# Kernel optimization log

Measured on AMD Instinct MI355X. Metric: run time of the kernel, lower is better.

The kernel has to match this reference:

```python
import jax, jax.numpy as jnp
import numpy as np

B, S, D = 4, 2048, 1024
H = 16
DH = D // H

def setup_inputs() -> dict:
    key = jax.random.key(0)
    ks = jax.random.split(key, 5)
    s = 1.0 / np.sqrt(D)
    return {
        "inputs": jax.random.normal(ks[0], (B, S, D), dtype=jnp.float32),
        "Wq": jax.random.normal(ks[1], (D, D), dtype=jnp.float32) * s,
        "Wk": jax.random.normal(ks[2], (D, D), dtype=jnp.float32) * s,
        "Wv": jax.random.normal(ks[3], (D, D), dtype=jnp.float32) * s,
        "Wo": jax.random.normal(ks[4], (D, D), dtype=jnp.float32) * s,
        "bo": jnp.zeros((D,), dtype=jnp.float32),
    }

def reference(inputs, Wq, Wk, Wv, Wo, bo):
    b, s, _ = inputs.shape
    # nn.Linear: y = x @ W.T (no bias for QKV)
    Q = (inputs @ Wq.T).reshape(b, s, H, DH)
    K = (inputs @ Wk.T).reshape(b, s, H, DH)
    V = (inputs @ Wv.T).reshape(b, s, H, DH)
    scores = jnp.einsum("bqhd,bkhd->bhqk", Q, K)  # [B,H,S,S]
    causal = jnp.triu(jnp.ones((s, s), dtype=bool), k=1)
    scores = jnp.where(causal, -jnp.inf, scores)
    w = jax.nn.softmax(scores / np.sqrt(DH), axis=-1)  # dropout p=0.0 -> identity
    Z = jnp.einsum("bhqk,bkhd->bqhd", w, V).reshape(b, s, D)
    return Z @ Wo.T + bo
```

## Files before the change

kernel.cpp:

```cpp
#include <hip/hip_runtime.h>
#include <hip/hip_bf16.h>


#define Bq 4
#define Sq 2048
#define Dq 1024
#define Hq 16
#define DHq 64

typedef __attribute__((ext_vector_type(8))) short short8;
typedef __attribute__((ext_vector_type(4))) float f32x4;
typedef __attribute__((ext_vector_type(4))) unsigned short ushort4v;
typedef __attribute__((ext_vector_type(2))) unsigned int uint2v;

static __device__ __forceinline__ unsigned short f2bfu(float f) {
    union { __hip_bfloat16 h; unsigned short u; } cv;
    cv.h = __float2bfloat16(f);
    return cv.u;
}
static __device__ __forceinline__ unsigned int cvtpk(float lo, float hi) {
    unsigned int r;
    asm("v_cvt_pk_bf16_f32 %0, %1, %2" : "=v"(r) : "v"(lo), "v"(hi));
    return r;
}

__global__ __launch_bounds__(256) void tobf16(
    const float* __restrict__ X, const float* __restrict__ W0,
    const float* __restrict__ W1, const float* __restrict__ W2,
    const float* __restrict__ W3,
    unsigned short* __restrict__ xb, unsigned short* __restrict__ wb)
{
    const size_t i = ((size_t)blockIdx.x * 256 + threadIdx.x) * 8;
    const size_t NX = (size_t)8388608;
    const float* src; unsigned short* dst; size_t off;
    if (i < NX) { src = X; dst = xb; off = i; }
    else {
        const size_t j = i - NX;
        const int w = (int)(j >> 20);
        off = j & 1048575;
        src = (w == 0) ? W0 : (w == 1) ? W1 : (w == 2) ? W2 : W3;
        dst = wb + ((size_t)w << 20);
    }
    const float4 a = *reinterpret_cast<const float4*>(src + off);
    const float4 b = *reinterpret_cast<const float4*>(src + off + 4);
    short8 v;
    v[0] = (short)f2bfu(a.x); v[1] = (short)f2bfu(a.y);
    v[2] = (short)f2bfu(a.z); v[3] = (short)f2bfu(a.w);
    v[4] = (short)f2bfu(b.x); v[5] = (short)f2bfu(b.y);
    v[6] = (short)f2bfu(b.z); v[7] = (short)f2bfu(b.w);
    *reinterpret_cast<short8*>(dst + off) = v;
}



__global__ __launch_bounds__(256) void mm_qkv(
    const unsigned short* __restrict__ Ab, const unsigned short* __restrict__ Wall,
    unsigned short* __restrict__ oq, unsigned short* __restrict__ ok,
    unsigned short* __restrict__ ovt)
{
    __shared__ unsigned short As[128 * 64];
    __shared__ unsigned short Bs[128 * 64];

    const int z = blockIdx.z;
    const unsigned short* W = Wall + ((size_t)z << 20);

    const int m0 = blockIdx.x * 128, n0 = blockIdx.y * 128;
    const int t = threadIdx.x, lane = t & 63, wave = t >> 6;
    const int g = lane >> 4, c = lane & 15;
    const int wm = wave >> 1, wn = wave & 1;
    const int r8 = lane >> 3, c8 = lane & 7;
    const int ss = (c8 ^ (r8 & 7)) * 8;

    f32x4 acc[4][4] = {};

    for (int kt = 0; kt < 16; ++kt) {
        const int kb = kt * 64;
#pragma unroll
        for (int p = 0; p < 4; ++p) {
            const int rowb = wave * 8 + p * 32;
            const unsigned short* ga = Ab + (size_t)(m0 + rowb + r8) * 1024 + kb + ss;
            const unsigned short* gb = W  + (size_t)(n0 + rowb + r8) * 1024 + kb + ss;
            __builtin_amdgcn_global_load_lds(
                (const __attribute__((address_space(1))) unsigned int*)ga,
                (__attribute__((address_space(3))) unsigned int*)(As + rowb * 64), 16, 0, 0);
            __builtin_amdgcn_global_load_lds(
                (const __attribute__((address_space(1))) unsigned int*)gb,
                (__attribute__((address_space(3))) unsigned int*)(Bs + rowb * 64), 16, 0, 0);
        }
        __syncthreads();
        if (z != 2) {
#pragma unroll
            for (int ks = 0; ks < 2; ++ks) {
                const int sa = ((ks * 4 + g) ^ (c & 7)) * 8;
                short8 bf[4];
#pragma unroll
                for (int nt = 0; nt < 4; ++nt)
                    bf[nt] = *reinterpret_cast<const short8*>(&Bs[(wn * 64 + nt * 16 + c) * 64 + sa]);
#pragma unroll
                for (int mt = 0; mt < 4; ++mt) {
                    const short8 af = *reinterpret_cast<const short8*>(&As[(wm * 64 + mt * 16 + c) * 64 + sa]);
#pragma unroll
                    for (int nt = 0; nt < 4; ++nt)
                        acc[mt][nt] = __builtin_amdgcn_mfma_f32_16x16x32_bf16(af, bf[nt], acc[mt][nt], 0, 0, 0);
                }
            }
        } else {
#pragma unroll
            for (int ks = 0; ks < 2; ++ks) {
                const int sa = ((ks * 4 + g) ^ (c & 7)) * 8;
                short8 bf[4];
#pragma unroll
                for (int nt = 0; nt < 4; ++nt)
                    bf[nt] = *reinterpret_cast<const short8*>(&Bs[(wn * 64 + nt * 16 + c) * 64 + sa]);
#pragma unroll
                for (int mt = 0; mt < 4; ++mt) {
                    const short8 af = *reinterpret_cast<const short8*>(&As[(wm * 64 + mt * 16 + c) * 64 + sa]);
#pragma unroll
                    for (int nt = 0; nt < 4; ++nt)
                        acc[mt][nt] = __builtin_amdgcn_mfma_f32_16x16x32_bf16(bf[nt], af, acc[mt][nt], 0, 0, 0);
                }
            }
        }
        __syncthreads();
    }

    if (z == 2) {
#pragma unroll
        for (int mt = 0; mt < 4; ++mt)
#pragma unroll
            for (int nt = 0; nt < 4; ++nt)
#pragma unroll
                for (int r = 0; r < 4; ++r) {
                    const int m = m0 + wm * 64 + mt * 16 + c;
                    const int n = n0 + wn * 64 + nt * 16 + g * 4 + r;
                    const int bb = m >> 11, s = m & 2047;
                    const int h = n >> 6, d = n & 63;
                    const size_t off = (size_t)(bb * Hq + h) * 131072
                        + (s >> 6) * 4096 + ((d >> 4) & 3) * 1024 + ((s >> 5) & 1) * 512
                        + ((s >> 3) & 3) * 128 + (d & 15) * 8 + (s & 7);
                    ovt[off] = f2bfu(acc[mt][nt][r]);
                }
    } else {
        const float oscale = (z == 0) ? 0.180336880f : 1.0f;
        unsigned short* out = z ? ok : oq;
#pragma unroll
        for (int mt = 0; mt < 4; ++mt)
#pragma unroll
            for (int nt = 0; nt < 4; ++nt)
#pragma unroll
                for (int r = 0; r < 4; ++r) {
                    const int m = m0 + wm * 64 + mt * 16 + g * 4 + r;
                    const int n = n0 + wn * 64 + nt * 16 + c;
                    const int bb = m >> 11, s = m & 2047;
                    const int h = n >> 6, d = n & 63;
                    const size_t off = (size_t)(bb * Hq + h) * 131072
                        + (s >> 4) * 1024 + (d >> 5) * 512 + ((d >> 3) & 3) * 128
                        + (s & 15) * 8 + (d & 7);
                    out[off] = f2bfu(acc[mt][nt][r] * oscale);
                }
    }
}

static __device__ __forceinline__ void stage_kv8(
    const unsigned short* __restrict__ Kb, const unsigned short* __restrict__ Vb,
    int kb, unsigned short* kl, unsigned short* vl, int wave, int lane)
{
    const int off = wave * 512 + lane * 8;
    __builtin_amdgcn_global_load_lds(
        (const __attribute__((address_space(1))) unsigned int*)(Kb + (size_t)kb * 4096 + off),
        (__attribute__((address_space(3))) unsigned int*)(kl + wave * 512), 16, 0, 0);
    __builtin_amdgcn_global_load_lds(
        (const __attribute__((address_space(1))) unsigned int*)(Vb + (size_t)kb * 4096 + off),
        (__attribute__((address_space(3))) unsigned int*)(vl + wave * 512), 16, 0, 0);
}

static __device__ __forceinline__ void pack_p(
    f32x4* st, int rel, int g, int c, unsigned short (*PtW)[72],
    short8& pb0, short8& pb1)
{
    if (rel < 4) {
        const int lim = rel * 16 + c;
#pragma unroll
        for (int kt = 0; kt < 4; ++kt)
#pragma unroll
            for (int r = 0; r < 4; ++r)
                if (kt * 16 + g * 4 + r > lim) st[kt][r] = -3.0e38f;
    }
#pragma unroll
    for (int kt = 0; kt < 4; ++kt) {
        uint2v u;
        u[0] = cvtpk(exp2f(st[kt][0]), exp2f(st[kt][1]));
        u[1] = cvtpk(exp2f(st[kt][2]), exp2f(st[kt][3]));
        *reinterpret_cast<uint2v*>(&PtW[c][kt * 16 + g * 4]) = u;
    }
    pb0 = *reinterpret_cast<const short8*>(&PtW[c][g * 8]);
    pb1 = *reinterpret_cast<const short8*>(&PtW[c][32 + g * 8]);
}

__global__ __launch_bounds__(512, 2) void attn(
    const unsigned short* __restrict__ Qf, const unsigned short* __restrict__ Kf,
    const unsigned short* __restrict__ Vf, unsigned short* __restrict__ O)
{
    __shared__ unsigned short Kl[2][4096];
    __shared__ unsigned short Vl[2][4096];
    __shared__ unsigned short Pt[8][16][72];

    const int bid = blockIdx.x;
    const int half = bid >> 8;
    const int idx = (bid >> 6) & 3;
    const int qq = half ? (3 - idx) : (4 + idx);
    const int bh = (bid & 7) | (((bid >> 3) & 7) << 3);

    const int t = threadIdx.x, lane = t & 63, wave = t >> 6;
    const int g = lane >> 4, c = lane & 15;
    const size_t base = (size_t)bh * (Sq * DHq);
    const unsigned short* Qb = Qf + base;
    const unsigned short* Kb = Kf + base;
    const unsigned short* Vb = Vf + base;
    const int b = bh >> 4, h = bh & 15;

    short8 onesf;
#pragma unroll
    for (int j = 0; j < 8; ++j) onesf[j] = (short)0x3F80;

    const int qtA = qq * 16 + wave * 2;
    const int qtB = qtA + 1;

    const unsigned short* qpA = Qb + (size_t)qtA * 1024 + lane * 8;
    const unsigned short* qpB = Qb + (size_t)qtB * 1024 + lane * 8;
    const short8 qA0 = *reinterpret_cast<const short8*>(qpA);
    const short8 qA1 = *reinterpret_cast<const short8*>(qpA + 512);
    const short8 qB0 = *reinterpret_cast<const short8*>(qpB);
    const short8 qB1 = *reinterpret_cast<const short8*>(qpB + 512);

    f32x4 oA[4] = {}, oB[4] = {};
    f32x4 lA = {}, lB = {};

    const int ibmax = 4 * qq + 3;

    stage_kv8(Kb, Vb, 0, Kl[0], Vl[0], wave, lane);
    __syncthreads();

#pragma unroll 1
    for (int ib = 0; ib <= ibmax; ++ib) {
        const int cur = ib & 1;
        if (ib < ibmax)
            stage_kv8(Kb, Vb, ib + 1, Kl[cur ^ 1], Vl[cur ^ 1], wave, lane);
        __builtin_amdgcn_sched_barrier(0);

        if (4 * ib <= qtA) {
            const unsigned short* kl = &Kl[cur][lane * 8];
            const unsigned short* vl = &Vl[cur][lane * 8];

            f32x4 stA[4] = {}, stB[4] = {};
#pragma unroll
            for (int k2 = 0; k2 < 4; ++k2) {
                const short8 kf0 = *reinterpret_cast<const short8*>(&kl[(2 * k2) * 512]);
                const short8 kf1 = *reinterpret_cast<const short8*>(&kl[(2 * k2 + 1) * 512]);
                stA[k2] = __builtin_amdgcn_mfma_f32_16x16x32_bf16(kf0, qA0, stA[k2], 0, 0, 0);
                stA[k2] = __builtin_amdgcn_mfma_f32_16x16x32_bf16(kf1, qA1, stA[k2], 0, 0, 0);
                stB[k2] = __builtin_amdgcn_mfma_f32_16x16x32_bf16(kf0, qB0, stB[k2], 0, 0, 0);
                stB[k2] = __builtin_amdgcn_mfma_f32_16x16x32_bf16(kf1, qB1, stB[k2], 0, 0, 0);
            }

            short8 pbA0, pbA1, pbB0, pbB1;
            pack_p(stA, qtA - 4 * ib, g, c, Pt[wave], pbA0, pbA1);
            pack_p(stB, qtB - 4 * ib, g, c, Pt[wave], pbB0, pbB1);

            lA = __builtin_amdgcn_mfma_f32_16x16x32_bf16(onesf, pbA0, lA, 0, 0, 0);
            lA = __builtin_amdgcn_mfma_f32_16x16x32_bf16(onesf, pbA1, lA, 0, 0, 0);
            lB = __builtin_amdgcn_mfma_f32_16x16x32_bf16(onesf, pbB0, lB, 0, 0, 0);
            lB = __builtin_amdgcn_mfma_f32_16x16x32_bf16(onesf, pbB1, lB, 0, 0, 0);

#pragma unroll
            for (int dt = 0; dt < 4; ++dt) {
                const short8 vf0 = *reinterpret_cast<const short8*>(&vl[(2 * dt) * 512]);
                const short8 vf1 = *reinterpret_cast<const short8*>(&vl[(2 * dt + 1) * 512]);
                oA[dt] = __builtin_amdgcn_mfma_f32_16x16x32_bf16(vf0, pbA0, oA[dt], 0, 0, 0);
                oA[dt] = __builtin_amdgcn_mfma_f32_16x16x32_bf16(vf1, pbA1, oA[dt], 0, 0, 0);
                oB[dt] = __builtin_amdgcn_mfma_f32_16x16x32_bf16(vf0, pbB0, oB[dt], 0, 0, 0);
                oB[dt] = __builtin_amdgcn_mfma_f32_16x16x32_bf16(vf1, pbB1, oB[dt], 0, 0, 0);
            }
        }
        __syncthreads();
    }

    const float rlA = 1.0f / lA[0];
    const float rlB = 1.0f / lB[0];
    const size_t orowA = ((size_t)b * Sq + qtA * 16 + c) * Dq + h * 64;
    const size_t orowB = ((size_t)b * Sq + qtB * 16 + c) * Dq + h * 64;
#pragma unroll
    for (int dt = 0; dt < 4; ++dt) {
        uint2v uA, uB;
        uA[0] = cvtpk(oA[dt][0] * rlA, oA[dt][1] * rlA);
        uA[1] = cvtpk(oA[dt][2] * rlA, oA[dt][3] * rlA);
        uB[0] = cvtpk(oB[dt][0] * rlB, oB[dt][1] * rlB);
        uB[1] = cvtpk(oB[dt][2] * rlB, oB[dt][3] * rlB);
        *reinterpret_cast<uint2v*>(&O[orowA + dt * 16 + g * 4]) = uA;
        *reinterpret_cast<uint2v*>(&O[orowB + dt * 16 + g * 4]) = uB;
    }
}

__global__ __launch_bounds__(256) void mm_o(
    const unsigned short* __restrict__ Ab, const unsigned short* __restrict__ Wall,
    const float* __restrict__ bo, float* __restrict__ outf)
{
    __shared__ unsigned short As[128 * 64];
    __shared__ unsigned short Bs[128 * 64];

    const unsigned short* W = Wall + ((size_t)3 << 20);

    const int m0 = blockIdx.x * 128, n0 = blockIdx.y * 128;
    const int t = threadIdx.x, lane = t & 63, wave = t >> 6;
    const int g = lane >> 4, c = lane & 15;
    const int wm = wave >> 1, wn = wave & 1;
    const int r8 = lane >> 3, c8 = lane & 7;
    const int ss = (c8 ^ (r8 & 7)) * 8;

    f32x4 acc[4][4] = {};

    for (int kt = 0; kt < 16; ++kt) {
        const int kb = kt * 64;
#pragma unroll
        for (int p = 0; p < 4; ++p) {
            const int rowb = wave * 8 + p * 32;
            const unsigned short* ga = Ab + (size_t)(m0 + rowb + r8) * 1024 + kb + ss;
            const unsigned short* gb = W  + (size_t)(n0 + rowb + r8) * 1024 + kb + ss;
            __builtin_amdgcn_global_load_lds(
                (const __attribute__((address_space(1))) unsigned int*)ga,
                (__attribute__((address_space(3))) unsigned int*)(As + rowb * 64), 16, 0, 0);
            __builtin_amdgcn_global_load_lds(
                (const __attribute__((address_space(1))) unsigned int*)gb,
                (__attribute__((address_space(3))) unsigned int*)(Bs + rowb * 64), 16, 0, 0);
        }
        __syncthreads();
#pragma unroll
        for (int ks = 0; ks < 2; ++ks) {
            const int sa = ((ks * 4 + g) ^ (c & 7)) * 8;
            short8 bf[4];
#pragma unroll
            for (int nt = 0; nt < 4; ++nt)
                bf[nt] = *reinterpret_cast<const short8*>(&Bs[(wn * 64 + nt * 16 + c) * 64 + sa]);
#pragma unroll
            for (int mt = 0; mt < 4; ++mt) {
                const short8 af = *reinterpret_cast<const short8*>(&As[(wm * 64 + mt * 16 + c) * 64 + sa]);
#pragma unroll
                for (int nt = 0; nt < 4; ++nt)
                    acc[mt][nt] = __builtin_amdgcn_mfma_f32_16x16x32_bf16(af, bf[nt], acc[mt][nt], 0, 0, 0);
            }
        }
        __syncthreads();
    }

#pragma unroll
    for (int nt = 0; nt < 4; ++nt) {
        const int n = n0 + wn * 64 + nt * 16 + c;
        const float bias = bo[n];
#pragma unroll
        for (int mt = 0; mt < 4; ++mt)
#pragma unroll
            for (int r = 0; r < 4; ++r) {
                const int m = m0 + wm * 64 + mt * 16 + g * 4 + r;
                outf[(size_t)m * 1024 + n] = acc[mt][nt][r] + bias;
            }
    }
}

extern "C" void kernel_launch(void* const* d_in, const int* in_sizes, int n_in,
                              void* d_out, int out_size, void* d_ws, size_t ws_size,
                              hipStream_t stream) {
    const float* X  = (const float*)d_in[0];
    const float* Wq = (const float*)d_in[1];
    const float* Wk = (const float*)d_in[2];
    const float* Wv = (const float*)d_in[3];
    const float* Wo = (const float*)d_in[4];
    const float* bo = (const float*)d_in[5];
    float* out = (float*)d_out;

    const size_t elems = (size_t)Bq * Hq * Sq * DHq;
    unsigned short* q  = (unsigned short*)d_ws;
    unsigned short* k  = q + elems;
    unsigned short* vt = k + elems;
    unsigned short* xo = vt + elems;
    unsigned short* wb = xo + elems;

    tobf16<<<dim3(6144), 256, 0, stream>>>(X, Wq, Wk, Wv, Wo, xo, wb);

    mm_qkv<<<dim3(64, 8, 3), 256, 0, stream>>>(xo, wb, q, k, vt);

    attn<<<dim3(512), 512, 0, stream>>>(q, k, vt, xo);

    mm_o<<<dim3(64, 8, 1), 256, 0, stream>>>(xo, wb, bo, out);
}
```

Before: 183.1 us.

## Replace GEMM kernels with 8-wave triple-buffered pipelined template for QKV and output

Both projection GEMMs are merged into one templated kernel that uses 512 threads and 256x128 tiles. Loads of the K tile two steps ahead go into a three-slot LDS ring using global_load_lds, with vmcnt waits and raw barriers in place of two __syncthreads per step. MFMA sections run at raised priority, and loads are split into two halves interleaved with compute. This aims to hide global-load latency and cut barrier stalls. In exchange it uses more LDS per block (one block per CU) and a larger tile, which reduces the block count for the output GEMM.

Result: slower. 209.6 us (+14.5%).

```diff
diff --git a/kernel.cpp b/kernel.cpp
--- a/kernel.cpp
+++ b/kernel.cpp
@@ -10,7 +10,6 @@
 
 typedef __attribute__((ext_vector_type(8))) short short8;
 typedef __attribute__((ext_vector_type(4))) float f32x4;
-typedef __attribute__((ext_vector_type(4))) unsigned short ushort4v;
 typedef __attribute__((ext_vector_type(2))) unsigned int uint2v;
 
 static __device__ __forceinline__ unsigned short f2bfu(float f) {
@@ -52,79 +51,146 @@
 }
 
 
-
-__global__ __launch_bounds__(256) void mm_qkv(
+template<int MODE>
+__global__ __launch_bounds__(512, 1) void mm8p(
     const unsigned short* __restrict__ Ab, const unsigned short* __restrict__ Wall,
     unsigned short* __restrict__ oq, unsigned short* __restrict__ ok,
-    unsigned short* __restrict__ ovt)
-{
-    __shared__ unsigned short As[128 * 64];
-    __shared__ unsigned short Bs[128 * 64];
-
-    const int z = blockIdx.z;
-    const unsigned short* W = Wall + ((size_t)z << 20);
-
-    const int m0 = blockIdx.x * 128, n0 = blockIdx.y * 128;
-    const int t = threadIdx.x, lane = t & 63, wave = t >> 6;
+    unsigned short* __restrict__ ovt, const float* __restrict__ bo,
+    float* __restrict__ outf)
+{
+    __shared__ unsigned short As[3][16384];
+    __shared__ unsigned short Bs[3][8192];
+
+    const int m0 = blockIdx.x * 256, n0g = blockIdx.y * 128;
+    const unsigned short* W = Wall + ((MODE == 0) ? (size_t)n0g * 1024
+                                                  : ((size_t)3 << 20) + (size_t)n0g * 1024);
+    const int z = (MODE == 0) ? (n0g >> 10) : 3;
+
+    const int tid = threadIdx.x, lane = tid & 63, wave = tid >> 6;
     const int g = lane >> 4, c = lane & 15;
     const int wm = wave >> 1, wn = wave & 1;
-    const int r8 = lane >> 3, c8 = lane & 7;
-    const int ss = (c8 ^ (r8 & 7)) * 8;
+    const int sr = tid >> 3;
+    const int ssw = ((tid & 7) ^ (sr & 7)) * 8;
 
     f32x4 acc[4][4] = {};
 
+#define STA(KT, SLOT, J)                                                        \
+    __builtin_amdgcn_global_load_lds(                                           \
+        (const __attribute__((address_space(1))) unsigned int*)(                \
+            Ab + (size_t)(m0 + (J) * 64 + sr) * 1024 + (KT) * 64 + ssw),        \
+        (__attribute__((address_space(3))) unsigned int*)(&As[SLOT][(J) * 4096 + wave * 512]), 16, 0, 0)
+#define STB(KT, SLOT, J)                                                        \
+    __builtin_amdgcn_global_load_lds(                                           \
+        (const __attribute__((address_space(1))) unsigned int*)(                \
+            W + (size_t)((J) * 64 + sr) * 1024 + (KT) * 64 + ssw),              \
+        (__attribute__((address_space(3))) unsigned int*)(&Bs[SLOT][(J) * 4096 + wave * 512]), 16, 0, 0)
+
+    STA(0, 0, 0); STA(0, 0, 1); STA(0, 0, 2); STA(0, 0, 3); STB(0, 0, 0); STB(0, 0, 1);
+    STA(1, 1, 0); STA(1, 1, 1); STA(1, 1, 2); STA(1, 1, 3); STB(1, 1, 0); STB(1, 1, 1);
+    asm volatile("s_waitcnt vmcnt(6)" ::: "memory");
+    __builtin_amdgcn_s_barrier();
+
+    int scur = 0;
+#pragma unroll 1
     for (int kt = 0; kt < 16; ++kt) {
-        const int kb = kt * 64;
-#pragma unroll
-        for (int p = 0; p < 4; ++p) {
-            const int rowb = wave * 8 + p * 32;
-            const unsigned short* ga = Ab + (size_t)(m0 + rowb + r8) * 1024 + kb + ss;
-            const unsigned short* gb = W  + (size_t)(n0 + rowb + r8) * 1024 + kb + ss;
-            __builtin_amdgcn_global_load_lds(
-                (const __attribute__((address_space(1))) unsigned int*)ga,
-                (__attribute__((address_space(3))) unsigned int*)(As + rowb * 64), 16, 0, 0);
-            __builtin_amdgcn_global_load_lds(
-                (const __attribute__((address_space(1))) unsigned int*)gb,
-                (__attribute__((address_space(3))) unsigned int*)(Bs + rowb * 64), 16, 0, 0);
+        const int snx2 = (scur >= 1) ? scur - 1 : scur + 2;
+        const unsigned short* Acur = As[scur];
+        const unsigned short* Bcur = Bs[scur];
+
+        if (kt < 14) { STA(kt + 2, snx2, 0); STA(kt + 2, snx2, 1); STB(kt + 2, snx2, 0); }
+        short8 bf[4][2];
+#pragma unroll
+        for (int nt = 0; nt < 4; ++nt)
+#pragma unroll
+            for (int ks = 0; ks < 2; ++ks)
+                bf[nt][ks] = *reinterpret_cast<const short8*>(
+                    &Bcur[(wn * 64 + nt * 16 + c) * 64 + ((ks * 4 + g) ^ (c & 7)) * 8]);
+        {
+            short8 af[2][2];
+#pragma unroll
+            for (int j = 0; j < 2; ++j)
+#pragma unroll
+                for (int ks = 0; ks < 2; ++ks)
+                    af[j][ks] = *reinterpret_cast<const short8*>(
+                        &Acur[(wm * 64 + j * 16 + c) * 64 + ((ks * 4 + g) ^ (c & 7)) * 8]);
+            __builtin_amdgcn_s_setprio(1);
+            if (MODE == 0 && z == 2) {
+#pragma unroll
+                for (int ks = 0; ks < 2; ++ks)
+#pragma unroll
+                    for (int j = 0; j < 2; ++j)
+#pragma unroll
+                        for (int nt = 0; nt < 4; ++nt)
+                            acc[j][nt] = __builtin_amdgcn_mfma_f32_16x16x32_bf16(
+                                bf[nt][ks], af[j][ks], acc[j][nt], 0, 0, 0);
+            } else {
+#pragma unroll
+                for (int ks = 0; ks < 2; ++ks)
+#pragma unroll
+                    for (int j = 0; j < 2; ++j)
+#pragma unroll
+                        for (int nt = 0; nt < 4; ++nt)
+                            acc[j][nt] = __builtin_amdgcn_mfma_f32_16x16x32_bf16(
+                                af[j][ks], bf[nt][ks], acc[j][nt], 0, 0, 0);
+            }
+            __builtin_amdgcn_s_setprio(0);
         }
-        __syncthreads();
-        if (z != 2) {
-#pragma unroll
-            for (int ks = 0; ks < 2; ++ks) {
-                const int sa = ((ks * 4 + g) ^ (c & 7)) * 8;
-                short8 bf[4];
-#pragma unroll
-                for (int nt = 0; nt < 4; ++nt)
-                    bf[nt] = *reinterpret_cast<const short8*>(&Bs[(wn * 64 + nt * 16 + c) * 64 + sa]);
-#pragma unroll
-                for (int mt = 0; mt < 4; ++mt) {
-                    const short8 af = *reinterpret_cast<const short8*>(&As[(wm * 64 + mt * 16 + c) * 64 + sa]);
-#pragma unroll
-                    for (int nt = 0; nt < 4; ++nt)
-                        acc[mt][nt] = __builtin_amdgcn_mfma_f32_16x16x32_bf16(af, bf[nt], acc[mt][nt], 0, 0, 0);
+        __builtin_amdgcn_s_barrier();
+
+        if (kt < 14) { STA(kt + 2, snx2, 2); STA(kt + 2, snx2, 3); STB(kt + 2, snx2, 1); }
+        {
+            short8 af[2][2];
+#pragma unroll
+            for (int j = 0; j < 2; ++j)
+#pragma unroll
+                for (int ks = 0; ks < 2; ++ks)
+                    af[j][ks] = *reinterpret_cast<const short8*>(
+                        &Acur[(wm * 64 + (2 + j) * 16 + c) * 64 + ((ks * 4 + g) ^ (c & 7)) * 8]);
+            __builtin_amdgcn_s_setprio(1);
+            if (MODE == 0 && z == 2) {
+#pragma unroll
+                for (int ks = 0; ks < 2; ++ks)
+#pragma unroll
+                    for (int j = 0; j < 2; ++j)
+#pragma unroll
+                        for (int nt = 0; nt < 4; ++nt)
+                            acc[2 + j][nt] = __builtin_amdgcn_mfma_f32_16x16x32_bf16(
+                                bf[nt][ks], af[j][ks], acc[2 + j][nt], 0, 0, 0);
+            } else {
+#pragma unroll
+                for (int ks = 0; ks < 2; ++ks)
+#pragma unroll
+                    for (int j = 0; j < 2; ++j)
+#pragma unroll
+                        for (int nt = 0; nt < 4; ++nt)
+                            acc[2 + j][nt] = __builtin_amdgcn_mfma_f32_16x16x32_bf16(
+                                af[j][ks], bf[nt][ks], acc[2 + j][nt], 0, 0, 0);
+            }
+            __builtin_amdgcn_s_setprio(0);
+        }
+        if (kt < 14)       asm volatile("s_waitcnt vmcnt(6)" ::: "memory");
+        else if (kt == 14) asm volatile("s_waitcnt vmcnt(0)" ::: "memory");
+        __builtin_amdgcn_s_barrier();
+
+        scur = (scur == 2) ? 0 : scur + 1;
+    }
+#undef STA
+#undef STB
+
+    if (MODE == 1) {
+#pragma unroll
+        for (int nt = 0; nt < 4; ++nt) {
+            const int n = n0g + wn * 64 + nt * 16 + c;
+            const float bias = bo[n];
+#pragma unroll
+            for (int mt = 0; mt < 4; ++mt)
+#pragma unroll
+                for (int r = 0; r < 4; ++r) {
+                    const int m = m0 + wm * 64 + mt * 16 + g * 4 + r;
+                    outf[(size_t)m * 1024 + n] = acc[mt][nt][r] + bias;
                 }
-            }
-        } else {
-#pragma unroll
-            for (int ks = 0; ks < 2; ++ks) {
-                const int sa = ((ks * 4 + g) ^ (c & 7)) * 8;
-                short8 bf[4];
-#pragma unroll
-                for (int nt = 0; nt < 4; ++nt)
-                    bf[nt] = *reinterpret_cast<const short8*>(&Bs[(wn * 64 + nt * 16 + c) * 64 + sa]);
-#pragma unroll
-                for (int mt = 0; mt < 4; ++mt) {
-                    const short8 af = *reinterpret_cast<const short8*>(&As[(wm * 64 + mt * 16 + c) * 64 + sa]);
-#pragma unroll
-                    for (int nt = 0; nt < 4; ++nt)
-                        acc[mt][nt] = __builtin_amdgcn_mfma_f32_16x16x32_bf16(bf[nt], af, acc[mt][nt], 0, 0, 0);
-                }
-            }
         }
-        __syncthreads();
-    }
-
-    if (z == 2) {
+    } else if (z == 2) {
 #pragma unroll
         for (int mt = 0; mt < 4; ++mt)
 #pragma unroll
@@ -132,9 +198,10 @@
 #pragma unroll
                 for (int r = 0; r < 4; ++r) {
                     const int m = m0 + wm * 64 + mt * 16 + c;
-                    const int n = n0 + wn * 64 + nt * 16 + g * 4 + r;
+                    const int n = n0g + wn * 64 + nt * 16 + g * 4 + r;
                     const int bb = m >> 11, s = m & 2047;
-                    const int h = n >> 6, d = n & 63;
+                    const int nn = n & 1023;
+                    const int h = nn >> 6, d = nn & 63;
                     const size_t off = (size_t)(bb * Hq + h) * 131072
                         + (s >> 6) * 4096 + ((d >> 4) & 3) * 1024 + ((s >> 5) & 1) * 512
                         + ((s >> 3) & 3) * 128 + (d & 15) * 8 + (s & 7);
@@ -150,9 +217,10 @@
 #pragma unroll
                 for (int r = 0; r < 4; ++r) {
                     const int m = m0 + wm * 64 + mt * 16 + g * 4 + r;
-                    const int n = n0 + wn * 64 + nt * 16 + c;
+                    const int n = n0g + wn * 64 + nt * 16 + c;
                     const int bb = m >> 11, s = m & 2047;
-                    const int h = n >> 6, d = n & 63;
+                    const int nn = n & 1023;
+                    const int h = nn >> 6, d = nn & 63;
                     const size_t off = (size_t)(bb * Hq + h) * 131072
                         + (s >> 4) * 1024 + (d >> 5) * 512 + ((d >> 3) & 3) * 128
                         + (s & 15) * 8 + (d & 7);
@@ -301,71 +369,6 @@
     }
 }
 
-__global__ __launch_bounds__(256) void mm_o(
-    const unsigned short* __restrict__ Ab, const unsigned short* __restrict__ Wall,
-    const float* __restrict__ bo, float* __restrict__ outf)
-{
-    __shared__ unsigned short As[128 * 64];
-    __shared__ unsigned short Bs[128 * 64];
-
-    const unsigned short* W = Wall + ((size_t)3 << 20);
-
-    const int m0 = blockIdx.x * 128, n0 = blockIdx.y * 128;
-    const int t = threadIdx.x, lane = t & 63, wave = t >> 6;
-    const int g = lane >> 4, c = lane & 15;
-    const int wm = wave >> 1, wn = wave & 1;
-    const int r8 = lane >> 3, c8 = lane & 7;
-    const int ss = (c8 ^ (r8 & 7)) * 8;
-
-    f32x4 acc[4][4] = {};
-
-    for (int kt = 0; kt < 16; ++kt) {
-        const int kb = kt * 64;
-#pragma unroll
-        for (int p = 0; p < 4; ++p) {
-            const int rowb = wave * 8 + p * 32;
-            const unsigned short* ga = Ab + (size_t)(m0 + rowb + r8) * 1024 + kb + ss;
-            const unsigned short* gb = W  + (size_t)(n0 + rowb + r8) * 1024 + kb + ss;
-            __builtin_amdgcn_global_load_lds(
-                (const __attribute__((address_space(1))) unsigned int*)ga,
-                (__attribute__((address_space(3))) unsigned int*)(As + rowb * 64), 16, 0, 0);
-            __builtin_amdgcn_global_load_lds(
-                (const __attribute__((address_space(1))) unsigned int*)gb,
-                (__attribute__((address_space(3))) unsigned int*)(Bs + rowb * 64), 16, 0, 0);
-        }
-        __syncthreads();
-#pragma unroll
-        for (int ks = 0; ks < 2; ++ks) {
-            const int sa = ((ks * 4 + g) ^ (c & 7)) * 8;
-            short8 bf[4];
-#pragma unroll
-            for (int nt = 0; nt < 4; ++nt)
-                bf[nt] = *reinterpret_cast<const short8*>(&Bs[(wn * 64 + nt * 16 + c) * 64 + sa]);
-#pragma unroll
-            for (int mt = 0; mt < 4; ++mt) {
-                const short8 af = *reinterpret_cast<const short8*>(&As[(wm * 64 + mt * 16 + c) * 64 + sa]);
-#pragma unroll
-                for (int nt = 0; nt < 4; ++nt)
-                    acc[mt][nt] = __builtin_amdgcn_mfma_f32_16x16x32_bf16(af, bf[nt], acc[mt][nt], 0, 0, 0);
-            }
-        }
-        __syncthreads();
-    }
-
-#pragma unroll
-    for (int nt = 0; nt < 4; ++nt) {
-        const int n = n0 + wn * 64 + nt * 16 + c;
-        const float bias = bo[n];
-#pragma unroll
-        for (int mt = 0; mt < 4; ++mt)
-#pragma unroll
-            for (int r = 0; r < 4; ++r) {
-                const int m = m0 + wm * 64 + mt * 16 + g * 4 + r;
-                outf[(size_t)m * 1024 + n] = acc[mt][nt][r] + bias;
-            }
-    }
-}
-
 extern "C" void kernel_launch(void* const* d_in, const int* in_sizes, int n_in,
                               void* d_out, int out_size, void* d_ws, size_t ws_size,
                               hipStream_t stream) {
@@ -386,9 +389,9 @@
 
     tobf16<<<dim3(6144), 256, 0, stream>>>(X, Wq, Wk, Wv, Wo, xo, wb);
 
-    mm_qkv<<<dim3(64, 8, 3), 256, 0, stream>>>(xo, wb, q, k, vt);
+    mm8p<0><<<dim3(32, 24), 512, 0, stream>>>(xo, wb, q, k, vt, nullptr, nullptr);
 
     attn<<<dim3(512), 512, 0, stream>>>(q, k, vt, xo);
 
-    mm_o<<<dim3(64, 8, 1), 256, 0, stream>>>(xo, wb, bo, out);
-}
+    mm8p<1><<<dim3(32, 8), 512, 0, stream>>>(xo, wb, nullptr, nullptr, nullptr, bo, out);
+}
```
